# Kernel tuning notes

Measured on AMD Instinct MI355X. Metric: run time of the kernel, lower is better.

## Reference

```python
import jax, jax.numpy as jnp
import numpy as np

N = 262144
D = 128  # hidden_dim
NUM_RULES = 5


def setup_inputs() -> dict:
    key = jax.random.key(0)
    ks = jax.random.split(key, 7)
    h_fused = jax.random.normal(ks[0], (N, D), dtype=jnp.float32)
    entity_types = jax.random.randint(ks[1], (N,), 0, 3)
    entity_masks = jnp.ones((N,), dtype=bool)
    # rule_scorer params (torch nn.Linear convention: y = x @ W.T + b)
    W1 = jax.random.normal(ks[2], (D, 3 * D), dtype=jnp.float32) * (1.0 / np.sqrt(3 * D))
    b1 = jnp.zeros((D,), dtype=jnp.float32)
    W2 = jax.random.normal(ks[3], (1, D), dtype=jnp.float32) * (1.0 / np.sqrt(D))
    b2 = jnp.zeros((1,), dtype=jnp.float32)
    rule_table = jax.random.normal(ks[4], (NUM_RULES, D), dtype=jnp.float32) * 0.1
    return {"h_fused": h_fused, "entity_types": entity_types,
            "entity_masks": entity_masks, "rule_id": 0,
            "W1": W1, "b1": b1, "W2": W2, "b2": b2, "rule_table": rule_table}


def reference(h_fused, entity_types, entity_masks, rule_id, W1, b1, W2, b2, rule_table):
    # masks per entity type
    car_mask = (entity_types == 0) & entity_masks
    light_mask = (entity_types == 1) & entity_masks
    stop_mask = (entity_types == 2) & entity_masks

    def masked_mean(mask):
        mf = mask.astype(h_fused.dtype)[:, None]            # [N,1]
        cnt = mf.sum()
        s = (h_fused * mf).sum(axis=0)                      # [D]
        return jnp.where(cnt > 0, s / jnp.maximum(cnt, 1.0), 0.0)

    h_light = masked_mean(light_mask)  # [D] - pooled once (original redundantly recomputes per car)
    h_stop = masked_mean(stop_mask)    # [D]

    n = h_fused.shape[0]
    concat = jnp.concatenate([
        h_fused,
        jnp.broadcast_to(h_light, (n, D)),
        jnp.broadcast_to(h_stop, (n, D)),
    ], axis=1)                                              # [N, 3D]

    hid = jax.nn.relu(concat @ W1.T + b1)                   # [N, D] (dropout = identity, eval)
    beta = jax.nn.sigmoid(hid @ W2.T + b2)[:, 0]            # [N]

    rule_emb = rule_table[rule_id]                          # [D]
    h_car = beta[:, None] * h_fused + (1.0 - beta[:, None]) * rule_emb
    h_out = jnp.where(car_mask[:, None], h_car, h_fused)    # [N, D]
    beta_out = jnp.where(car_mask, beta, 0.0)               # [N]; original compacts to [N_car]
    return h_out, beta_out
```

## Files before the change

### kernel.cpp

```cpp
#include <hip/hip_runtime.h>
#include <hip/hip_bf16.h>

#define D 128

typedef __attribute__((ext_vector_type(8))) short short8;
typedef __attribute__((ext_vector_type(4))) float f32x4;

__device__ __forceinline__ unsigned short f2bf(float f) {
  unsigned int u = __float_as_uint(f);
  u += 0x7FFFu + ((u >> 16) & 1u);
  return (unsigned short)(u >> 16);
}

__device__ __forceinline__ bool mask_at(const unsigned char* m, int i, bool i32layout) {
  return i32layout ? (((const int*)m)[i] != 0) : (m[i] != 0);
}


__global__ __launch_bounds__(256) void k_reduce(
    const float* __restrict__ h, const int* __restrict__ types,
    const unsigned char* __restrict__ masks, float* __restrict__ ws) {
  const int t = threadIdx.x;
  const int c4 = t & 31;
  const int rgrp = t >> 5;
  const int row0 = blockIdx.x * 256;
  const bool mi32 = (masks[1] == 0);
  __shared__ float wl_s[256], ws_s[256];
  __shared__ float redL[8][128], redS[8][128];
  {
    const int r = row0 + t;
    const int ty = types[r];
    const bool m = mask_at(masks, r, mi32);
    wl_s[t] = (ty == 1 && m) ? 1.f : 0.f;
    ws_s[t] = (ty == 2 && m) ? 1.f : 0.f;
  }
  __syncthreads();
  f32x4 sl = {0.f, 0.f, 0.f, 0.f}, ss = {0.f, 0.f, 0.f, 0.f};
  #pragma unroll 4
  for (int i = 0; i < 32; ++i) {
    const int rl = rgrp + 8 * i;
    const f32x4 v = *(const f32x4*)&h[(size_t)(row0 + rl) * D + c4 * 4];
    const float wl = wl_s[rl];
    const float w2 = ws_s[rl];
    sl += v * wl;
    ss += v * w2;
  }
  *(f32x4*)&redL[rgrp][c4 * 4] = sl;
  *(f32x4*)&redS[rgrp][c4 * 4] = ss;
  __syncthreads();
  {
    const int arr = t >> 7, col = t & 127;
    float s = 0.f;
    #pragma unroll
    for (int g = 0; g < 8; ++g) s += arr ? redS[g][col] : redL[g][col];
    atomicAdd(&ws[arr * 128 + col], s);
  }
  if (t < 64) {
    float c = wl_s[t] + wl_s[t + 64] + wl_s[t + 128] + wl_s[t + 192];
    #pragma unroll
    for (int m = 1; m < 64; m <<= 1) c += __shfl_xor(c, m, 64);
    if (t == 0) atomicAdd(&ws[256], c);
  } else if (t < 128) {
    const int u = t - 64;
    float c = ws_s[u] + ws_s[u + 64] + ws_s[u + 128] + ws_s[u + 192];
    #pragma unroll
    for (int m = 1; m < 64; m <<= 1) c += __shfl_xor(c, m, 64);
    if (t == 64) atomicAdd(&ws[257], c);
  }
}

__global__ __launch_bounds__(256) void k_prep(
    const float* __restrict__ W1, const float* __restrict__ b1,
    float* __restrict__ ws) {
  const int b = blockIdx.x;
  const int t = threadIdx.x;
  unsigned short* w1abf = (unsigned short*)(ws + 512);
  {
    const int idx = b * 256 + t;
    const int j = idx >> 7, k = idx & 127;
    w1abf[idx] = f2bf(W1[j * 384 + k]);
  }
  const int half = t >> 7, k = t & 127;
  const int j = b * 2 + half;
  const float cl = ws[256], cs = ws[257];
  const float hlk = (cl > 0.f) ? ws[k] / cl : 0.f;
  const float hsk = (cs > 0.f) ? ws[D + k] / cs : 0.f;
  float v = hlk * W1[j * 384 + 128 + k] + hsk * W1[j * 384 + 256 + k];
  #pragma unroll
  for (int m = 1; m < 64; m <<= 1) v += __shfl_xor(v, m, 64);
  __shared__ float red[4];
  if ((t & 63) == 0) red[t >> 6] = v;
  __syncthreads();
  if (t == 0) {
    ws[258 + b * 2 + 0] = red[0] + red[1] + b1[b * 2 + 0];
    ws[258 + b * 2 + 1] = red[2] + red[3] + b1[b * 2 + 1];
  }
}

__global__ __launch_bounds__(256, 2) void k_main(
    const float* __restrict__ h, const int* __restrict__ types,
    const unsigned char* __restrict__ masks,
    const int* __restrict__ rid_p,
    const float* __restrict__ W2, const float* __restrict__ b2p,
    const float* __restrict__ rule_table,
    const float* __restrict__ ws,
    float* __restrict__ out_h, float* __restrict__ out_beta) {
  __shared__ unsigned short Bs[128][136];
  __shared__ unsigned short As[64][136];
  __shared__ float cs_s[128], w2_s[128], rule_s[128];
  __shared__ float betas[64], car_s[64];

  const int t = threadIdx.x;
  const int wave = t >> 6;
  const int lane = t & 63;
  const int lrow = lane & 15;
  const int q = lane >> 4;
  const bool mi32 = (masks[1] == 0);
  const unsigned short* w1abf = (const unsigned short*)(ws + 512);
  const float* cvec = ws + 258;

  {
    const int rid = rid_p[0];
    if (t < 128) {
      cs_s[t] = cvec[t];
      rule_s[t] = rule_table[rid * D + t];
    } else {
      w2_s[t - 128] = W2[t - 128];
    }
    #pragma unroll
    for (int i = 0; i < 8; ++i) {
      const int flat = i * 256 + t;
      const int row = flat >> 4;
      const int c8 = flat & 15;
      *(uint4*)&Bs[row][c8 * 8] = *(const uint4*)&w1abf[flat * 8];
    }
  }
  __syncthreads();

  short8 breg[32];
  #pragma unroll
  for (int i = 0; i < 32; ++i) {
    const int nt = i >> 2, ks = i & 3;
    breg[i] = *(const short8*)&Bs[nt * 16 + lrow][ks * 32 + q * 8];
  }
  const float b2v = b2p[0];

  for (int tile = 0; tile < 4; ++tile) {
    const int row0 = (blockIdx.x * 4 + tile) * 64;
    #pragma unroll
    for (int i = 0; i < 8; ++i) {
      const int flat = i * 256 + t;
      const int r = flat >> 5, c4 = flat & 31;
      const f32x4 v = *(const f32x4*)&h[(size_t)(row0 + r) * D + c4 * 4];
      ushort4 bv;
      bv.x = f2bf(v.x); bv.y = f2bf(v.y); bv.z = f2bf(v.z); bv.w = f2bf(v.w);
      *(ushort4*)&As[r][c4 * 4] = bv;
    }
    __syncthreads();

    if (t < 64) {
      const int grow = row0 + t;
      car_s[t] = ((types[grow] == 0) && mask_at(masks, grow, mi32)) ? 1.f : 0.f;
    }

    short8 a[4];
    #pragma unroll
    for (int ks = 0; ks < 4; ++ks)
      a[ks] = *(const short8*)&As[wave * 16 + lrow][ks * 32 + q * 8];

    f32x4 acc[8];
    #pragma unroll
    for (int nt = 0; nt < 8; ++nt) acc[nt] = (f32x4){0.f, 0.f, 0.f, 0.f};
    #pragma unroll
    for (int nt = 0; nt < 8; ++nt) {
      #pragma unroll
      for (int ks = 0; ks < 4; ++ks)
        acc[nt] = __builtin_amdgcn_mfma_f32_16x16x32_bf16(a[ks], breg[nt * 4 + ks], acc[nt], 0, 0, 0);
    }

    float part[4] = {0.f, 0.f, 0.f, 0.f};
    #pragma unroll
    for (int nt = 0; nt < 8; ++nt) {
      const int col = nt * 16 + lrow;
      const float cv = cs_s[col];
      const float wv = w2_s[col];
      #pragma unroll
      for (int r = 0; r < 4; ++r)
        part[r] += fmaxf(acc[nt][r] + cv, 0.f) * wv;
    }
    #pragma unroll
    for (int m = 1; m < 16; m <<= 1) {
      #pragma unroll
      for (int r = 0; r < 4; ++r) part[r] += __shfl_xor(part[r], m, 64);
    }
    if (lrow == 0) {
      #pragma unroll
      for (int r = 0; r < 4; ++r) {
        const float z = part[r] + b2v;
        betas[wave * 16 + q * 4 + r] = 1.f / (1.f + __expf(-z));
      }
    }
    __syncthreads();

    #pragma unroll
    for (int i = 0; i < 4; ++i) {
      const int flat8 = i * 256 + t;
      const int r = flat8 >> 4, c8 = flat8 & 15;
      const uint4 u = *(const uint4*)&As[r][c8 * 8];
      const float beta = betas[r];
      const float cf = car_s[r];
      const float a_r = cf * beta + (1.f - cf);
      const float b_r = cf * (1.f - beta);
      f32x4 o0, o1;
      o0.x = a_r * __uint_as_float(u.x << 16)          + b_r * rule_s[c8 * 8 + 0];
      o0.y = a_r * __uint_as_float(u.x & 0xFFFF0000u)  + b_r * rule_s[c8 * 8 + 1];
      o0.z = a_r * __uint_as_float(u.y << 16)          + b_r * rule_s[c8 * 8 + 2];
      o0.w = a_r * __uint_as_float(u.y & 0xFFFF0000u)  + b_r * rule_s[c8 * 8 + 3];
      o1.x = a_r * __uint_as_float(u.z << 16)          + b_r * rule_s[c8 * 8 + 4];
      o1.y = a_r * __uint_as_float(u.z & 0xFFFF0000u)  + b_r * rule_s[c8 * 8 + 5];
      o1.z = a_r * __uint_as_float(u.w << 16)          + b_r * rule_s[c8 * 8 + 6];
      o1.w = a_r * __uint_as_float(u.w & 0xFFFF0000u)  + b_r * rule_s[c8 * 8 + 7];
      float* op = &out_h[(size_t)(row0 + r) * D + c8 * 8];
      *(f32x4*)op = o0;
      *(f32x4*)(op + 4) = o1;
    }
    if (t < 64) out_beta[row0 + t] = car_s[t] * betas[t];
    __syncthreads();
  }
}

extern "C" void kernel_launch(void* const* d_in, const int* in_sizes, int n_in,
                              void* d_out, int out_size, void* d_ws, size_t ws_size,
                              hipStream_t stream) {
  const float* h = (const float*)d_in[0];
  const int* types = (const int*)d_in[1];
  const unsigned char* masks = (const unsigned char*)d_in[2];
  const int* rid = (const int*)d_in[3];
  const float* W1 = (const float*)d_in[4];
  const float* b1 = (const float*)d_in[5];
  const float* W2 = (const float*)d_in[6];
  const float* b2 = (const float*)d_in[7];
  const float* rule_table = (const float*)d_in[8];
  float* ws = (float*)d_ws;
  const int n = in_sizes[0] / D;
  float* out_h = (float*)d_out;
  float* out_beta = out_h + (size_t)n * D;

  hipMemsetAsync(d_ws, 0, 258 * sizeof(float), stream);
  k_reduce<<<n / 256, 256, 0, stream>>>(h, types, masks, ws);
  k_prep<<<64, 256, 0, stream>>>(W1, b1, ws);
  k_main<<<n / 256, 256, 0, stream>>>(h, types, masks, rid, W2, b2, rule_table, ws,
                                      out_h, out_beta);
}
```

Baseline: 301.1 us.

## Load activations directly into MFMA registers and drop LDS staging and block barriers

The main kernel no longer stages each 64-row tile of h through shared memory. Each wave now loads its own 16 rows straight into MFMA A-fragment registers. Beta is redistributed with wave shuffles, and each lane writes its output row from registers, which removes the per-tile __syncthreads and LDS round trips. Bias, W2 and rule-embedding vectors are kept in registers instead of LDS. The cost is more register pressure and global access patterns that are less coalesced (each lane reads 8 floats per ks chunk, spread over rows), and output stores are strided the same way.

```diff
diff --git a/kernel.cpp b/kernel.cpp
--- a/kernel.cpp
+++ b/kernel.cpp
@@ -10,6 +10,9 @@
   unsigned int u = __float_as_uint(f);
   u += 0x7FFFu + ((u >> 16) & 1u);
   return (unsigned short)(u >> 16);
+}
+__device__ __forceinline__ float bf2f(short s) {
+  return __uint_as_float(((unsigned int)(unsigned short)s) << 16);
 }
 
 __device__ __forceinline__ bool mask_at(const unsigned char* m, int i, bool i32layout) {
@@ -106,9 +109,6 @@
     const float* __restrict__ ws,
     float* __restrict__ out_h, float* __restrict__ out_beta) {
   __shared__ unsigned short Bs[128][136];
-  __shared__ unsigned short As[64][136];
-  __shared__ float cs_s[128], w2_s[128], rule_s[128];
-  __shared__ float betas[64], car_s[64];
 
   const int t = threadIdx.x;
   const int wave = t >> 6;
@@ -119,21 +119,12 @@
   const unsigned short* w1abf = (const unsigned short*)(ws + 512);
   const float* cvec = ws + 258;
 
-  {
-    const int rid = rid_p[0];
-    if (t < 128) {
-      cs_s[t] = cvec[t];
-      rule_s[t] = rule_table[rid * D + t];
-    } else {
-      w2_s[t - 128] = W2[t - 128];
-    }
-    #pragma unroll
-    for (int i = 0; i < 8; ++i) {
-      const int flat = i * 256 + t;
-      const int row = flat >> 4;
-      const int c8 = flat & 15;
-      *(uint4*)&Bs[row][c8 * 8] = *(const uint4*)&w1abf[flat * 8];
-    }
+  #pragma unroll
+  for (int i = 0; i < 8; ++i) {
+    const int flat = i * 256 + t;
+    const int row = flat >> 4;
+    const int c8 = flat & 15;
+    *(uint4*)&Bs[row][c8 * 8] = *(const uint4*)&w1abf[flat * 8];
   }
   __syncthreads();
 
@@ -143,30 +134,37 @@
     const int nt = i >> 2, ks = i & 3;
     breg[i] = *(const short8*)&Bs[nt * 16 + lrow][ks * 32 + q * 8];
   }
+
+  float creg[8], w2reg[8];
+  #pragma unroll
+  for (int nt = 0; nt < 8; ++nt) {
+    creg[nt] = cvec[nt * 16 + lrow];
+    w2reg[nt] = W2[nt * 16 + lrow];
+  }
+  f32x4 rr[8];
+  {
+    const int rid = rid_p[0];
+    #pragma unroll
+    for (int ks = 0; ks < 4; ++ks) {
+      rr[2 * ks]     = *(const f32x4*)&rule_table[rid * D + ks * 32 + q * 8];
+      rr[2 * ks + 1] = *(const f32x4*)&rule_table[rid * D + ks * 32 + q * 8 + 4];
+    }
+  }
   const float b2v = b2p[0];
 
   for (int tile = 0; tile < 4; ++tile) {
-    const int row0 = (blockIdx.x * 4 + tile) * 64;
-    #pragma unroll
-    for (int i = 0; i < 8; ++i) {
-      const int flat = i * 256 + t;
-      const int r = flat >> 5, c4 = flat & 31;
-      const f32x4 v = *(const f32x4*)&h[(size_t)(row0 + r) * D + c4 * 4];
-      ushort4 bv;
-      bv.x = f2bf(v.x); bv.y = f2bf(v.y); bv.z = f2bf(v.z); bv.w = f2bf(v.w);
-      *(ushort4*)&As[r][c4 * 4] = bv;
-    }
-    __syncthreads();
-
-    if (t < 64) {
-      const int grow = row0 + t;
-      car_s[t] = ((types[grow] == 0) && mask_at(masks, grow, mi32)) ? 1.f : 0.f;
-    }
+    const int row0 = blockIdx.x * 256 + wave * 64 + tile * 16;
+    const int grow = row0 + lrow;
+    const float* hrow = &h[(size_t)grow * D];
 
     short8 a[4];
     #pragma unroll
-    for (int ks = 0; ks < 4; ++ks)
-      a[ks] = *(const short8*)&As[wave * 16 + lrow][ks * 32 + q * 8];
+    for (int ks = 0; ks < 4; ++ks) {
+      const f32x4 v0 = *(const f32x4*)&hrow[ks * 32 + q * 8];
+      const f32x4 v1 = *(const f32x4*)&hrow[ks * 32 + q * 8 + 4];
+      a[ks] = (short8){(short)f2bf(v0.x), (short)f2bf(v0.y), (short)f2bf(v0.z), (short)f2bf(v0.w),
+                       (short)f2bf(v1.x), (short)f2bf(v1.y), (short)f2bf(v1.z), (short)f2bf(v1.w)};
+    }
 
     f32x4 acc[8];
     #pragma unroll
@@ -181,9 +179,8 @@
     float part[4] = {0.f, 0.f, 0.f, 0.f};
     #pragma unroll
     for (int nt = 0; nt < 8; ++nt) {
-      const int col = nt * 16 + lrow;
-      const float cv = cs_s[col];
-      const float wv = w2_s[col];
+      const float cv = creg[nt];
+      const float wv = w2reg[nt];
       #pragma unroll
       for (int r = 0; r < 4; ++r)
         part[r] += fmaxf(acc[nt][r] + cv, 0.f) * wv;
@@ -193,39 +190,41 @@
       #pragma unroll
       for (int r = 0; r < 4; ++r) part[r] += __shfl_xor(part[r], m, 64);
     }
-    if (lrow == 0) {
-      #pragma unroll
-      for (int r = 0; r < 4; ++r) {
-        const float z = part[r] + b2v;
-        betas[wave * 16 + q * 4 + r] = 1.f / (1.f + __expf(-z));
-      }
-    }
-    __syncthreads();
-
-    #pragma unroll
-    for (int i = 0; i < 4; ++i) {
-      const int flat8 = i * 256 + t;
-      const int r = flat8 >> 4, c8 = flat8 & 15;
-      const uint4 u = *(const uint4*)&As[r][c8 * 8];
-      const float beta = betas[r];
-      const float cf = car_s[r];
-      const float a_r = cf * beta + (1.f - cf);
-      const float b_r = cf * (1.f - beta);
+    float sig[4];
+    #pragma unroll
+    for (int r = 0; r < 4; ++r)
+      sig[r] = 1.f / (1.f + __expf(-(part[r] + b2v)));
+
+    const int src = (lrow >> 2) << 4;
+    const float g0 = __shfl(sig[0], src, 64);
+    const float g1 = __shfl(sig[1], src, 64);
+    const float g2 = __shfl(sig[2], src, 64);
+    const float g3 = __shfl(sig[3], src, 64);
+    const int s = lrow & 3;
+    const float beta = (s & 2) ? ((s & 1) ? g3 : g2) : ((s & 1) ? g1 : g0);
+
+    const bool car = (types[grow] == 0) && mask_at(masks, grow, mi32);
+    const float cf = car ? 1.f : 0.f;
+    const float a_r = cf * beta + (1.f - cf);
+    const float b_r = cf * (1.f - beta);
+
+    float* op = &out_h[(size_t)grow * D];
+    #pragma unroll
+    for (int ks = 0; ks < 4; ++ks) {
       f32x4 o0, o1;
-      o0.x = a_r * __uint_as_float(u.x << 16)          + b_r * rule_s[c8 * 8 + 0];
-      o0.y = a_r * __uint_as_float(u.x & 0xFFFF0000u)  + b_r * rule_s[c8 * 8 + 1];
-      o0.z = a_r * __uint_as_float(u.y << 16)          + b_r * rule_s[c8 * 8 + 2];
-      o0.w = a_r * __uint_as_float(u.y & 0xFFFF0000u)  + b_r * rule_s[c8 * 8 + 3];
-      o1.x = a_r * __uint_as_float(u.z << 16)          + b_r * rule_s[c8 * 8 + 4];
-      o1.y = a_r * __uint_as_float(u.z & 0xFFFF0000u)  + b_r * rule_s[c8 * 8 + 5];
-      o1.z = a_r * __uint_as_float(u.w << 16)          + b_r * rule_s[c8 * 8 + 6];
-      o1.w = a_r * __uint_as_float(u.w & 0xFFFF0000u)  + b_r * rule_s[c8 * 8 + 7];
-      float* op = &out_h[(size_t)(row0 + r) * D + c8 * 8];
-      *(f32x4*)op = o0;
-      *(f32x4*)(op + 4) = o1;
-    }
-    if (t < 64) out_beta[row0 + t] = car_s[t] * betas[t];
-    __syncthreads();
+      const f32x4 r0 = rr[2 * ks], r1 = rr[2 * ks + 1];
+      o0.x = a_r * bf2f(a[ks][0]) + b_r * r0.x;
+      o0.y = a_r * bf2f(a[ks][1]) + b_r * r0.y;
+      o0.z = a_r * bf2f(a[ks][2]) + b_r * r0.z;
+      o0.w = a_r * bf2f(a[ks][3]) + b_r * r0.w;
+      o1.x = a_r * bf2f(a[ks][4]) + b_r * r1.x;
+      o1.y = a_r * bf2f(a[ks][5]) + b_r * r1.y;
+      o1.z = a_r * bf2f(a[ks][6]) + b_r * r1.z;
+      o1.w = a_r * bf2f(a[ks][7]) + b_r * r1.w;
+      *(f32x4*)&op[ks * 32 + q * 8] = o0;
+      *(f32x4*)&op[ks * 32 + q * 8 + 4] = o1;
+    }
+    if (q == 0) out_beta[grow] = cf * beta;
   }
 }
 
```

Measured after the change: 316.1 us. 1.05x slower.
